# Optimization experiments

Hardware: AMD Instinct MI355X
Metric: run time of the kernel (lower is better)

## Reference

```python
import jax, jax.numpy as jnp
import numpy as np

HUMAN_SIZE = 54
NUM_ACTIONS = 15
INPUT_SIZE = HUMAN_SIZE + NUM_ACTIONS  # 69
RNN_SIZE = 2048
BATCH = 512
SRC_LEN = 100
TGT_LEN = 50


def setup_inputs() -> dict:
    key = jax.random.key(0)
    ks = jax.random.split(key, 8)
    s = 1.0 / np.sqrt(RNN_SIZE)
    return {
        "encoder_inputs": jax.random.normal(ks[0], (BATCH, SRC_LEN, INPUT_SIZE), jnp.float32),
        "decoder_inputs": jax.random.normal(ks[1], (BATCH, TGT_LEN, INPUT_SIZE), jnp.float32),
        # GRUCell params (torch layout: weight_ih [3H, D], weight_hh [3H, H])
        "W_ih": jax.random.uniform(ks[2], (3 * RNN_SIZE, INPUT_SIZE), jnp.float32, -s, s),
        "W_hh": jax.random.uniform(ks[3], (3 * RNN_SIZE, RNN_SIZE), jnp.float32, -s, s),
        "b_ih": jax.random.uniform(ks[4], (3 * RNN_SIZE,), jnp.float32, -s, s),
        "b_hh": jax.random.uniform(ks[5], (3 * RNN_SIZE,), jnp.float32, -s, s),
        # fc1: Linear(rnn_size -> input_size)
        "fc1_w": jax.random.uniform(ks[6], (INPUT_SIZE, RNN_SIZE), jnp.float32, -s, s),
        "fc1_b": jax.random.uniform(ks[7], (INPUT_SIZE,), jnp.float32, -s, s),
    }


def _gru_cell(x, h, W_ih, W_hh, b_ih, b_hh):
    # torch.nn.GRUCell math
    gi = x @ W_ih.T + b_ih  # [B, 3H]
    gh = h @ W_hh.T + b_hh  # [B, 3H]
    i_r, i_z, i_n = jnp.split(gi, 3, axis=-1)
    h_r, h_z, h_n = jnp.split(gh, 3, axis=-1)
    r = jax.nn.sigmoid(i_r + h_r)
    z = jax.nn.sigmoid(i_z + h_z)
    n = jnp.tanh(i_n + r * h_n)
    return (1.0 - z) * n + z * h


def reference(encoder_inputs, decoder_inputs, W_ih, W_hh, b_ih, b_hh, fc1_w, fc1_b):
    B = encoder_inputs.shape[0]
    state0 = jnp.zeros((B, RNN_SIZE), encoder_inputs.dtype)

    # Encoder: source_seq_len - 1 steps (dropout p=0.0 -> identity)
    enc_t = jnp.swapaxes(encoder_inputs[:, : SRC_LEN - 1], 0, 1)  # [L-1, B, D]

    def enc_step(h, x):
        return _gru_cell(x, h, W_ih, W_hh, b_ih, b_hh), None

    state, _ = jax.lax.scan(enc_step, state0, enc_t)

    # (loop_function feeds the previous output back as the next input).
    def dec_step(carry, _):
        h, inp = carry
        inp = jax.lax.stop_gradient(inp)  # inp.detach() in torch
        h = _gru_cell(inp, h, W_ih, W_hh, b_ih, b_hh)
        out = inp + h @ fc1_w.T + fc1_b  # residual
        return (h, out), out

    (_, _), outs = jax.lax.scan(dec_step, (state, decoder_inputs[:, 0]), None, length=TGT_LEN)
    return jnp.swapaxes(outs, 0, 1)  # [B, TGT_LEN, INPUT_SIZE]
```

## Files before the change

kernel.cpp:

```cpp
#include <hip/hip_runtime.h>

#define KP   2176
#define H    2048
#define IN   69
#define TGT  50
#define NKT  68

typedef unsigned short ushort_t;
typedef unsigned int   uint_t;
typedef __attribute__((ext_vector_type(8))) short  short8;
typedef __attribute__((ext_vector_type(4))) float  float4_t;

#define MFMA_BF16 __builtin_amdgcn_mfma_f32_16x16x32_bf16

__device__ __forceinline__ ushort_t f2bf(float f) {
  union { float f; unsigned u; } v; v.f = f;
  unsigned u = v.u;
  return (ushort_t)((u + 0x7fffu + ((u >> 16) & 1u)) >> 16);
}

template <int N> __device__ __forceinline__ void waitv() {
  asm volatile("s_waitcnt vmcnt(%0)" :: "n"(N) : "memory");
}
#define SGB0() __builtin_amdgcn_sched_barrier(0)

template <int OFF> __device__ __forceinline__ void gld(short8& d, uint_t voff, const void* base) {
  asm volatile("global_load_dwordx4 %0, %1, %2 offset:%3"
               : "=v"(d) : "v"(voff), "s"(base), "n"(OFF));
}


__global__ void build_w3(const float* __restrict__ Whh, const float* __restrict__ Wih,
                         ushort_t* __restrict__ W3) {
  int i = blockIdx.x * 256 + threadIdx.x;
  int lane = i & 63;
  int kt = (i >> 6) % NKT;
  int rb = i / (64 * NKT);
  int cb = rb / 3, g = rb - cb * 3;
  int c  = cb * 16 + (lane & 15);
  int gr = g * H + c;
  int k0 = kt * 32 + (lane >> 4) * 8;
  short8 v;
  #pragma unroll
  for (int j = 0; j < 8; ++j) {
    int k = k0 + j;
    float val = 0.f;
    if (k < H) val = Whh[(size_t)gr * H + k];
    else if (k < H + IN) val = Wih[(size_t)gr * IN + (k - H)];
    v[j] = (short)f2bf(val);
  }
  *(short8*)(W3 + (size_t)i * 8) = v;
}

__global__ void build_f2(const float* __restrict__ fc1w, ushort_t* __restrict__ F2) {
  int i = blockIdx.x * 256 + threadIdx.x;
  int lane = i & 63;
  int ni = (i >> 6) % 5;
  int kt = i / 320;
  int j  = ni * 16 + (lane & 15);
  int k0 = kt * 32 + (lane >> 4) * 8;
  short8 v;
  #pragma unroll
  for (int jj = 0; jj < 8; ++jj) {
    float val = (j < IN) ? fc1w[(size_t)j * H + k0 + jj] : 0.f;
    v[jj] = (short)f2bf(val);
  }
  *(short8*)(F2 + (size_t)i * 8) = v;
}

__global__ void zero_u4(uint4* p, int n) {
  int i = blockIdx.x * 256 + threadIdx.x;
  if (i < n) p[i] = make_uint4(0, 0, 0, 0);
}

__device__ __forceinline__ size_t a2_x_off(int b, int j) {
  int k = 2048 + j;
  int kt = k >> 5, kk = k & 31;
  int mb = b >> 4;
  int ln = (b & 15) | ((kk >> 3) << 4);
  return ((size_t)(mb * NKT + kt) * 64 + ln) * 16 + (kk & 7) * 2;
}

__global__ void fill_x0(const float* __restrict__ enc, char* __restrict__ A2) {
  int i = blockIdx.x * 256 + threadIdx.x;
  int b = i / IN, j = i - b * IN;
  *(ushort_t*)(A2 + a2_x_off(b, j)) = f2bf(enc[(size_t)b * 100 * IN + j]);
}

__global__ __launch_bounds__(256, 1) void gru_step(
    const char* __restrict__ Aprev, char* __restrict__ Anext,
    const char* __restrict__ W3p, float* __restrict__ h32,
    const float* __restrict__ bih, const float* __restrict__ bhh,
    const float* __restrict__ xsrc, int xstride)
{
  __shared__ __align__(16) char ldsbuf[90112];
  ushort_t (*smh)[72] = (ushort_t (*)[72])ldsbuf;

  const int tid = threadIdx.x;
  const int bid = blockIdx.x;
  const int lane = tid & 63, w = tid >> 6;
  const int l15 = lane & 15, l4 = lane >> 4;
  const int cg = (bid & 7) * 4 + ((bid >> 3) & 3);
  const int mt = bid >> 5;
  const int cb = cg * 4 + w;
  const int c  = cb * 16 + l15;

  const float br  = bih[c] + bhh[c];
  const float bz  = bih[H + c] + bhh[H + c];
  const float bin = bih[2 * H + c];
  const float bhn = bhh[2 * H + c];
  asm volatile("" :: "v"(br), "v"(bz), "v"(bin), "v"(bhn));

  const void* ApB0 = Aprev + (size_t)(mt * 4 + 0) * (NKT * 1024);
  const void* ApB1 = Aprev + (size_t)(mt * 4 + 1) * (NKT * 1024);
  const void* ApB2 = Aprev + (size_t)(mt * 4 + 2) * (NKT * 1024);
  const void* ApB3 = Aprev + (size_t)(mt * 4 + 3) * (NKT * 1024);
  uint_t vA  = (uint_t)(lane * 16);
  uint_t vB0 = (uint_t)((cb * 3 + 0) * (NKT * 1024) + lane * 16);
  uint_t vB1 = (uint_t)((cb * 3 + 1) * (NKT * 1024) + lane * 16);
  uint_t vB2 = (uint_t)((cb * 3 + 2) * (NKT * 1024) + lane * 16);

  short8 fa[8][4], fb[8][3];
  float4_t acc[4][4] = {};

#define ISSB(sl) \
  gld<0>(fb[sl][0], vB0, W3p); gld<0>(fb[sl][1], vB1, W3p); gld<0>(fb[sl][2], vB2, W3p); \
  vB0 += 1024; vB1 += 1024; vB2 += 1024;
#define ISSA(sl) \
  gld<0>(fa[sl][0], vA, ApB0); gld<0>(fa[sl][1], vA, ApB1); \
  gld<0>(fa[sl][2], vA, ApB2); gld<0>(fa[sl][3], vA, ApB3); \
  vA += 1024;
#define MFMAS(j, G2) \
  { _Pragma("unroll") \
    for (int mi = 0; mi < 4; ++mi) { \
      acc[mi][0]  = MFMA_BF16(fa[j][mi], fb[j][0], acc[mi][0], 0, 0, 0); \
      acc[mi][1]  = MFMA_BF16(fa[j][mi], fb[j][1], acc[mi][1], 0, 0, 0); \
      acc[mi][G2] = MFMA_BF16(fa[j][mi], fb[j][2], acc[mi][G2], 0, 0, 0); } }
#define GSUB(j, G2)  waitv<49>(); SGB0(); MFMAS(j, G2) ISSB(j) ISSA(j)
#define GSUBT(j, G2, N)  waitv<N>(); SGB0(); MFMAS(j, G2)

  ISSB(0) ISSA(0) ISSB(1) ISSA(1) ISSB(2) ISSA(2) ISSB(3) ISSA(3)
  ISSB(4) ISSA(4) ISSB(5) ISSA(5) ISSB(6) ISSA(6) ISSB(7) ISSA(7)

  #pragma unroll 1
  for (int s0 = 0; s0 < 56; s0 += 8) {
    GSUB(0, 2) GSUB(1, 2) GSUB(2, 2) GSUB(3, 2)
    GSUB(4, 2) GSUB(5, 2) GSUB(6, 2) GSUB(7, 2)
  }
  GSUB(0, 2) GSUB(1, 2) GSUB(2, 2) GSUB(3, 2)
  GSUBT(4, 2, 49) GSUBT(5, 2, 42) GSUBT(6, 2, 35) GSUBT(7, 2, 28)
  GSUBT(0, 3, 21) GSUBT(1, 3, 14) GSUBT(2, 3, 7)  GSUBT(3, 3, 0)

  #pragma unroll
  for (int mi = 0; mi < 4; ++mi) {
    #pragma unroll
    for (int r4 = 0; r4 < 4; ++r4) {
      int m = mt * 64 + mi * 16 + l4 * 4 + r4;
      float rg = 1.f / (1.f + __expf(-(acc[mi][0][r4] + br)));
      float zg = 1.f / (1.f + __expf(-(acc[mi][1][r4] + bz)));
      float ng = tanhf(acc[mi][3][r4] + bin + rg * (acc[mi][2][r4] + bhn));
      float hold = h32[(size_t)m * H + c];
      float hn = (1.f - zg) * ng + zg * hold;
      h32[(size_t)m * H + c] = hn;
      smh[mi * 16 + l4 * 4 + r4][w * 16 + l15] = f2bf(hn);
    }
  }
  __syncthreads();
  #pragma unroll
  for (int e = 0; e < 2; ++e) {
    int cid = tid * 2 + e;
    int m = cid >> 3, ktrel = (cid >> 2) & 1, khi = cid & 3;
    short8 v = *(const short8*)&smh[m][ktrel * 32 + khi * 8];
    int m_abs = mt * 64 + m;
    int mb2 = m_abs >> 4;
    int ln = (m_abs & 15) | (khi << 4);
    int kt = cg * 2 + ktrel;
    *(short8*)(Anext + ((size_t)(mb2 * NKT + kt) * 64 + ln) * 16) = v;
  }
  if ((bid & 31) == 0 && xsrc != nullptr) {
    for (int i = tid; i < 64 * IN; i += 256) {
      int rr = i / IN, cc = i - rr * IN;
      int m = mt * 64 + rr;
      *(ushort_t*)(Anext + a2_x_off(m, cc)) = f2bf(xsrc[(size_t)m * xstride + cc]);
    }
  }
}

__global__ __launch_bounds__(256, 1) void out_step(
    char* __restrict__ Acat, const char* __restrict__ F2p,
    const float* __restrict__ fc1b, const float* __restrict__ inp,
    float* __restrict__ outp)
{
  __shared__ float4_t redf[4 * 5 * 64];
  const int tid = threadIdx.x;
  const int mb = blockIdx.x;
  const int lane = tid & 63, w = tid >> 6;
  const int l15 = lane & 15, l4 = lane >> 4;

  const void* F2b = (const char*)F2p + 4096;
  uint_t voA = (uint_t)((mb * NKT + w * 16) * 1024 + lane * 16);
  uint_t vf  = (uint_t)((w * 16) * 5120 + lane * 16);

  short8 da[8], db[8][5];
  float4_t oa[5] = {};

#define DPRO(sl) \
  gld<0>(da[sl], voA, Acat); \
  gld<0>(db[sl][0], vf, F2p); gld<1024>(db[sl][1], vf, F2p); \
  gld<2048>(db[sl][2], vf, F2p); gld<3072>(db[sl][3], vf, F2p); \
  gld<0>(db[sl][4], vf, F2b); \
  voA += 1024; vf += 5120;
#define DMM(sl) \
  { _Pragma("unroll") for (int nf = 0; nf < 5; ++nf) \
      oa[nf] = MFMA_BF16(da[sl], db[sl][nf], oa[nf], 0, 0, 0); }

  DPRO(0) DPRO(1) DPRO(2) DPRO(3) DPRO(4) DPRO(5) DPRO(6) DPRO(7)
  waitv<42>(); SGB0(); DMM(0) DPRO(0)
  waitv<42>(); SGB0(); DMM(1) DPRO(1)
  waitv<42>(); SGB0(); DMM(2) DPRO(2)
  waitv<42>(); SGB0(); DMM(3) DPRO(3)
  waitv<42>(); SGB0(); DMM(4) DPRO(4)
  waitv<42>(); SGB0(); DMM(5) DPRO(5)
  waitv<42>(); SGB0(); DMM(6) DPRO(6)
  waitv<42>(); SGB0(); DMM(7) DPRO(7)
  waitv<42>(); SGB0(); DMM(0)
  waitv<36>(); SGB0(); DMM(1)
  waitv<30>(); SGB0(); DMM(2)
  waitv<24>(); SGB0(); DMM(3)
  waitv<18>(); SGB0(); DMM(4)
  waitv<12>(); SGB0(); DMM(5)
  waitv<6>();  SGB0(); DMM(6)
  waitv<0>();  SGB0(); DMM(7)

  #pragma unroll
  for (int nf = 0; nf < 5; ++nf) redf[(w * 5 + nf) * 64 + lane] = oa[nf];
  __syncthreads();

  #pragma unroll 1
  for (int pass = 0; pass < 2; ++pass) {
    if (pass == 1 && w != 0) break;
    const int nf = pass ? 4 : w;
    float4_t sum = redf[(0 * 5 + nf) * 64 + lane] + redf[(1 * 5 + nf) * 64 + lane]
                 + redf[(2 * 5 + nf) * 64 + lane] + redf[(3 * 5 + nf) * 64 + lane];
    int j = nf * 16 + l15;
    if (j < IN) {
      float bj = fc1b[j];
      #pragma unroll
      for (int r4 = 0; r4 < 4; ++r4) {
        int m = mb * 16 + l4 * 4 + r4;
        float v = sum[r4] + bj + inp[(size_t)m * (TGT * IN) + j];
        outp[(size_t)m * (TGT * IN) + j] = v;
        *(ushort_t*)(Acat + a2_x_off(m, j)) = f2bf(v);
      }
    }
  }
}

extern "C" void kernel_launch(void* const* d_in, const int* in_sizes, int n_in,
                              void* d_out, int out_size, void* d_ws, size_t ws_size,
                              hipStream_t stream) {
  const float* enc  = (const float*)d_in[0];
  const float* dec  = (const float*)d_in[1];
  const float* Wih  = (const float*)d_in[2];
  const float* Whh  = (const float*)d_in[3];
  const float* b_ih = (const float*)d_in[4];
  const float* b_hh = (const float*)d_in[5];
  const float* fc1w = (const float*)d_in[6];
  const float* fc1b = (const float*)d_in[7];
  float* out = (float*)d_out;

  char* ws = (char*)d_ws;
  ushort_t* W3  = (ushort_t*)ws;
  char*     A0  = ws + 26738688;
  char*     A1  = ws + 28966912;
  float*    h32 = (float*)(ws + 31195136);
  ushort_t* F2  = (ushort_t*)(ws + 35389440);
  char* A2[2] = {A0, A1};

  build_w3<<<6528, 256, 0, stream>>>(Whh, Wih, W3);
  zero_u4<<<2112, 256, 0, stream>>>((uint4*)A0, 540672);
  fill_x0<<<138, 256, 0, stream>>>(enc, A0);
  build_f2<<<80, 256, 0, stream>>>(fc1w, F2);

  for (int t = 0; t < 149; ++t) {
    const float* xsrc = nullptr; int xstride = 0;
    if (t < 98)       { xsrc = enc + (size_t)(t + 1) * IN; xstride = 100 * IN; }
    else if (t == 98) { xsrc = dec;                        xstride = TGT * IN; }
    gru_step<<<256, 256, 0, stream>>>(A2[t & 1], A2[(t + 1) & 1], (const char*)W3, h32,
                                      b_ih, b_hh, xsrc, xstride);
    if (t >= 99) {
      int d = t - 99;
      const float* inp = (d == 0) ? dec : out + (size_t)(d - 1) * IN;
      out_step<<<32, 256, 0, stream>>>(A2[(t + 1) & 1], (const char*)F2, fc1b, inp,
                                       out + (size_t)d * IN);
    }
  }
}
```

Before: 4.193 ms.

## Share A-operand tiles across waves through an LDS ring buffer

Previously every wave loaded all four A (hidden-state) fragments from global memory per k-step, so the four waves of a block fetched the same data four times. Now each wave loads one quarter of the A tile, writes it to a 4-slot LDS ring, and after a block barrier all waves read the full A tile from LDS. This cuts global/L2 traffic for A by four and frees registers from the deep A prefetch. The cost is a workgroup barrier and LDS round-trip on every k-step, with a shallower prefetch pipeline that may expose latency.

Result: faster. 4.024 ms (-4.0%).

```diff
diff --git a/kernel.cpp b/kernel.cpp
--- a/kernel.cpp
+++ b/kernel.cpp
@@ -22,7 +22,9 @@
 template <int N> __device__ __forceinline__ void waitv() {
   asm volatile("s_waitcnt vmcnt(%0)" :: "n"(N) : "memory");
 }
-#define SGB0() __builtin_amdgcn_sched_barrier(0)
+#define LGKM0() asm volatile("s_waitcnt lgkmcnt(0)" ::: "memory")
+#define SGB0()  __builtin_amdgcn_sched_barrier(0)
+#define FENCE() asm volatile("" ::: "memory")
 
 template <int OFF> __device__ __forceinline__ void gld(short8& d, uint_t voff, const void* base) {
   asm volatile("global_load_dwordx4 %0, %1, %2 offset:%3"
@@ -93,8 +95,9 @@
     const float* __restrict__ bih, const float* __restrict__ bhh,
     const float* __restrict__ xsrc, int xstride)
 {
-  __shared__ __align__(16) char ldsbuf[90112];
-  ushort_t (*smh)[72] = (ushort_t (*)[72])ldsbuf;
+  __shared__ short8  Aring[4][4][64];
+  __shared__ ushort_t smh[64][72];
+  __shared__ char ldspad[64000];
 
   const int tid = threadIdx.x;
   const int bid = blockIdx.x;
@@ -105,51 +108,89 @@
   const int cb = cg * 4 + w;
   const int c  = cb * 16 + l15;
 
+  if (xstride == -12345) ldspad[tid] = 1;
+
   const float br  = bih[c] + bhh[c];
   const float bz  = bih[H + c] + bhh[H + c];
   const float bin = bih[2 * H + c];
   const float bhn = bhh[2 * H + c];
   asm volatile("" :: "v"(br), "v"(bz), "v"(bin), "v"(bhn));
 
-  const void* ApB0 = Aprev + (size_t)(mt * 4 + 0) * (NKT * 1024);
-  const void* ApB1 = Aprev + (size_t)(mt * 4 + 1) * (NKT * 1024);
-  const void* ApB2 = Aprev + (size_t)(mt * 4 + 2) * (NKT * 1024);
-  const void* ApB3 = Aprev + (size_t)(mt * 4 + 3) * (NKT * 1024);
-  uint_t vA  = (uint_t)(lane * 16);
+  const void* ApW = Aprev + (size_t)(mt * 4) * (NKT * 1024);
+  uint_t vA  = (uint_t)(w * (NKT * 1024) + lane * 16);
   uint_t vB0 = (uint_t)((cb * 3 + 0) * (NKT * 1024) + lane * 16);
   uint_t vB1 = (uint_t)((cb * 3 + 1) * (NKT * 1024) + lane * 16);
   uint_t vB2 = (uint_t)((cb * 3 + 2) * (NKT * 1024) + lane * 16);
 
-  short8 fa[8][4], fb[8][3];
+  short8 sa[4], fb[8][3];
+  short8 fa0, fa1, fa2, fa3;
   float4_t acc[4][4] = {};
 
-#define ISSB(sl) \
-  gld<0>(fb[sl][0], vB0, W3p); gld<0>(fb[sl][1], vB1, W3p); gld<0>(fb[sl][2], vB2, W3p); \
-  vB0 += 1024; vB1 += 1024; vB2 += 1024;
-#define ISSA(sl) \
-  gld<0>(fa[sl][0], vA, ApB0); gld<0>(fa[sl][1], vA, ApB1); \
-  gld<0>(fa[sl][2], vA, ApB2); gld<0>(fa[sl][3], vA, ApB3); \
-  vA += 1024;
-#define MFMAS(j, G2) \
-  { _Pragma("unroll") \
-    for (int mi = 0; mi < 4; ++mi) { \
-      acc[mi][0]  = MFMA_BF16(fa[j][mi], fb[j][0], acc[mi][0], 0, 0, 0); \
-      acc[mi][1]  = MFMA_BF16(fa[j][mi], fb[j][1], acc[mi][1], 0, 0, 0); \
-      acc[mi][G2] = MFMA_BF16(fa[j][mi], fb[j][2], acc[mi][G2], 0, 0, 0); } }
-#define GSUB(j, G2)  waitv<49>(); SGB0(); MFMAS(j, G2) ISSB(j) ISSA(j)
-#define GSUBT(j, G2, N)  waitv<N>(); SGB0(); MFMAS(j, G2)
-
-  ISSB(0) ISSA(0) ISSB(1) ISSA(1) ISSB(2) ISSA(2) ISSB(3) ISSA(3)
-  ISSB(4) ISSA(4) ISSB(5) ISSA(5) ISSB(6) ISSA(6) ISSB(7) ISSA(7)
+#define AISS(sl) { gld<0>(sa[sl], vA, ApW); vA += 1024; }
+#define BISS(sl) { gld<0>(fb[sl][0], vB0, W3p); gld<0>(fb[sl][1], vB1, W3p); \
+                   gld<0>(fb[sl][2], vB2, W3p); vB0 += 1024; vB1 += 1024; vB2 += 1024; }
+#define MFMA3(mi, fav, j, G2) \
+  acc[mi][0]  = MFMA_BF16(fav, fb[j][0], acc[mi][0], 0, 0, 0); \
+  acc[mi][1]  = MFMA_BF16(fav, fb[j][1], acc[mi][1], 0, 0, 0); \
+  acc[mi][G2] = MFMA_BF16(fav, fb[j][2], acc[mi][G2], 0, 0, 0);
+#define MFMA12(j, G2) MFMA3(0, fa0, j, G2) MFMA3(1, fa1, j, G2) \
+                      MFMA3(2, fa2, j, G2) MFMA3(3, fa3, j, G2)
+#define RDFA(slot) \
+  FENCE(); \
+  fa0 = Aring[slot][0][lane]; fa1 = Aring[slot][1][lane]; \
+  fa2 = Aring[slot][2][lane]; fa3 = Aring[slot][3][lane];
+
+#define GRUT(u, G2) \
+  AISS((u + 4) & 3) BISS((u + 7) & 7) \
+  waitv<15>(); SGB0(); \
+  Aring[(u + 1) & 3][w][lane] = sa[(u + 1) & 3]; \
+  LGKM0(); \
+  __builtin_amdgcn_s_barrier(); \
+  RDFA(u & 3) \
+  LGKM0(); SGB0(); \
+  MFMA12(u, G2)
+
+#define GRUTA(u, NW) \
+  AISS((u + 4) & 3) \
+  waitv<NW>(); SGB0(); \
+  Aring[(u + 1) & 3][w][lane] = sa[(u + 1) & 3]; \
+  LGKM0(); \
+  __builtin_amdgcn_s_barrier(); \
+  RDFA(u & 3) \
+  LGKM0(); SGB0(); \
+  MFMA12(u, 2)
+
+#define GRUTN_W(u, NW, G2) \
+  waitv<NW>(); SGB0(); \
+  Aring[(u + 1) & 3][w][lane] = sa[(u + 1) & 3]; \
+  LGKM0(); \
+  __builtin_amdgcn_s_barrier(); \
+  RDFA(u & 3) \
+  LGKM0(); SGB0(); \
+  MFMA12(u, G2)
+#define GRUTN_NW(u, NW, G2) \
+  waitv<NW>(); SGB0(); \
+  LGKM0(); \
+  __builtin_amdgcn_s_barrier(); \
+  RDFA(u & 3) \
+  LGKM0(); SGB0(); \
+  MFMA12(u, G2)
+
+  AISS(0) AISS(1) AISS(2) AISS(3)
+  BISS(0) BISS(1) BISS(2) BISS(3) BISS(4) BISS(5) BISS(6)
+  waitv<24>(); SGB0();
+  Aring[0][w][lane] = sa[0];
+  LGKM0();
+  __builtin_amdgcn_s_barrier();
 
   #pragma unroll 1
-  for (int s0 = 0; s0 < 56; s0 += 8) {
-    GSUB(0, 2) GSUB(1, 2) GSUB(2, 2) GSUB(3, 2)
-    GSUB(4, 2) GSUB(5, 2) GSUB(6, 2) GSUB(7, 2)
-  }
-  GSUB(0, 2) GSUB(1, 2) GSUB(2, 2) GSUB(3, 2)
-  GSUBT(4, 2, 49) GSUBT(5, 2, 42) GSUBT(6, 2, 35) GSUBT(7, 2, 28)
-  GSUBT(0, 3, 21) GSUBT(1, 3, 14) GSUBT(2, 3, 7)  GSUBT(3, 3, 0)
+  for (int g8 = 0; g8 < 7; ++g8) {
+    GRUT(0, 2) GRUT(1, 2) GRUT(2, 2) GRUT(3, 2)
+    GRUT(4, 2) GRUT(5, 2) GRUT(6, 2) GRUT(7, 2)
+  }
+  GRUT(0, 2) GRUT(1, 2) GRUT(2, 2) GRUT(3, 2) GRUT(4, 2)
+  GRUTA(5, 12) GRUTA(6, 9) GRUTA(7, 6)
+  GRUTN_W(0, 2, 3) GRUTN_W(1, 1, 3) GRUTN_W(2, 0, 3) GRUTN_NW(3, 0, 3)
 
   #pragma unroll
   for (int mi = 0; mi < 4; ++mi) {
```
